# Performance work log

Measured on AMD Instinct MI355X. Metric: run time of the kernel, lower is better.

The kernel has to match this reference:

```python
import jax, jax.numpy as jnp
import numpy as np

# init_kwargs constants
K = 5                      # kernel_sz
SIGMA_SPATIAL = 2.0
SIGMA_INTENSITY = 0.1
KVAL = -1.0 / (2.0 * SIGMA_SPATIAL ** 2)        # kernel buffer value (same for all k^2 taps)
SIDIV = 1.0 / (2.0 * SIGMA_INTENSITY ** 2)      # sigma_intensity_div


def _extract_block(x, k):
    """F.unfold equivalent: (B,C,H,W) -> (B,H,W,k*k,C), SAME zero padding, row-major taps."""
    B, C, H, W = x.shape
    p = k // 2
    xp = jnp.pad(x, ((0, 0), (0, 0), (p, p), (p, p)))
    # fixed small loop over k*k taps (not a data-dim loop)
    pats = jnp.stack([xp[:, :, i:i + H, j:j + W] for i in range(k) for j in range(k)], axis=2)  # B,C,k2,H,W
    return jnp.transpose(pats, (0, 3, 4, 2, 1))  # B,H,W,k2,C


def setup_inputs() -> dict:
    key = jax.random.key(0)
    k1, k2 = jax.random.split(key)
    template = jax.random.uniform(k1, (1, 3, 1080, 1920), dtype=jnp.float32)
    vector_curr = jax.random.normal(k2, (1, 2, 1080, 1920), dtype=jnp.float32)
    return {"template": template, "vector_curr": vector_curr}


def reference(template, vector_curr):
    # inputs are float32, so cast() is a no-op
    compare_pix = jnp.transpose(template, (0, 2, 3, 1))[:, :, :, None, :]   # B,H,W,1,C
    compare_kernel = _extract_block(template, K)                            # B,H,W,k2,C
    intensity_diff = jnp.sum((compare_pix - compare_kernel) ** 2, axis=-1)  # B,H,W,k2
    coeff = jnp.clip(1.0 - jnp.abs(KVAL - intensity_diff * SIDIV), 0.0, 1.0)[..., None]  # B,H,W,k2,1
    vector_block = _extract_block(vector_curr, K)                           # B,H,W,k2,Cv
    num = jnp.sum(vector_block * coeff, axis=-2)                            # B,H,W,Cv
    den = jnp.sum(coeff, axis=-2)                                           # B,H,W,1
    out = (num / den).astype(jnp.float16)
    return jnp.transpose(out, (0, 3, 1, 2))                                  # B,Cv,H,W fp16
```

## Files before the change

kernel.cpp:

```cpp
#include <hip/hip_runtime.h>


#define IMG_H 1080
#define IMG_W 1920
#define IMG_HW (IMG_H * IMG_W)
#define TS_X 64
#define TS_Y 16
#define HALO_H 20
#define HALO_W 72
#define NCH 5
#define F4_PER_ROW 18
#define F4_PER_CH  (F4_PER_ROW * HALO_H)

typedef float f4u __attribute__((ext_vector_type(4), aligned(4)));

__global__ __launch_bounds__(256)
void jbf_kernel(const float* __restrict__ tpl,
                const float* __restrict__ vec,
                float* __restrict__ out) {
    constexpr float KVAL  = -0.125f;
    constexpr float SIDIV = 50.0f;

    __shared__ __align__(16) float smem[NCH][HALO_H][HALO_W];

    const int tid = threadIdx.x;
    const int x0  = blockIdx.x * TS_X;
    const int y0  = blockIdx.y * TS_Y;

    const bool interior = (blockIdx.x >= 1) & (blockIdx.x <= 28) &
                          (blockIdx.y >= 1) & (blockIdx.y <= 66);

    if (interior) {
        const int i0  = tid;
        const int i1  = tid + 256;
        const bool p1 = (i1 < F4_PER_CH);
        const int i1c = p1 ? i1 : 0;
        const int r0 = i0 / F4_PER_ROW, c0 = i0 - r0 * F4_PER_ROW;
        const int r1 = i1c / F4_PER_ROW, c1 = i1c - r1 * F4_PER_ROW;
        const int off0 = r0 * IMG_W + c0 * 4;
        const int off1 = r1 * IMG_W + c1 * 4;
        const int tl   = (y0 - 2) * IMG_W + (x0 - 2);

        f4u v[2 * NCH];
#pragma unroll
        for (int ch = 0; ch < NCH; ++ch) {
            const float* __restrict__ src =
                (ch < 3) ? (tpl + ch * IMG_HW) : (vec + (ch - 3) * IMG_HW);
            v[2 * ch]     = *(const f4u*)(src + tl + off0);
            v[2 * ch + 1] = *(const f4u*)(src + tl + off1);
        }
#pragma unroll
        for (int ch = 0; ch < NCH; ++ch) {
            float4* d0 = (float4*)&smem[ch][r0][c0 * 4];
            d0->x = v[2 * ch].x; d0->y = v[2 * ch].y;
            d0->z = v[2 * ch].z; d0->w = v[2 * ch].w;
            if (p1) {
                float4* d1 = (float4*)&smem[ch][r1][c1 * 4];
                d1->x = v[2 * ch + 1].x; d1->y = v[2 * ch + 1].y;
                d1->z = v[2 * ch + 1].z; d1->w = v[2 * ch + 1].w;
            }
        }
    } else {
#pragma unroll
        for (int c = 0; c < NCH; ++c) {
            const float* __restrict__ src =
                (c < 3) ? (tpl + c * IMG_HW) : (vec + (c - 3) * IMG_HW);
#pragma unroll
            for (int i = tid; i < HALO_H * HALO_W; i += 256) {
                const int r   = i / HALO_W;
                const int col = i - r * HALO_W;
                const int gy  = y0 + r - 2;
                const int gx  = x0 + col - 2;
                float val = 0.0f;
                if (gy >= 0 && gy < IMG_H && gx >= 0 && gx < IMG_W)
                    val = src[gy * IMG_W + gx];
                smem[c][r][col] = val;
            }
        }
    }
    __syncthreads();

    const int tx = tid & 15;
    const int ty = tid >> 4;
    const int lx = tx * 4;

    float num0[4] = {0.f, 0.f, 0.f, 0.f};
    float num1[4] = {0.f, 0.f, 0.f, 0.f};
    float den [4] = {0.f, 0.f, 0.f, 0.f};

    float c0[4], c1[4], c2[4];
#pragma unroll
    for (int px = 0; px < 4; ++px) {
        c0[px] = smem[0][ty + 2][lx + 2 + px];
        c1[px] = smem[1][ty + 2][lx + 2 + px];
        c2[px] = smem[2][ty + 2][lx + 2 + px];
    }

#pragma unroll
    for (int dy = 0; dy < 5; ++dy) {
        const int row = ty + dy;
        float4 a0 = *(const float4*)&smem[0][row][lx];
        float4 b0 = *(const float4*)&smem[0][row][lx + 4];
        float4 a1 = *(const float4*)&smem[1][row][lx];
        float4 b1 = *(const float4*)&smem[1][row][lx + 4];
        float4 a2 = *(const float4*)&smem[2][row][lx];
        float4 b2 = *(const float4*)&smem[2][row][lx + 4];
        float4 av0 = *(const float4*)&smem[3][row][lx];
        float4 bv0 = *(const float4*)&smem[3][row][lx + 4];
        float4 av1 = *(const float4*)&smem[4][row][lx];
        float4 bv1 = *(const float4*)&smem[4][row][lx + 4];

        const float w0[8]  = {a0.x, a0.y, a0.z, a0.w, b0.x, b0.y, b0.z, b0.w};
        const float w1[8]  = {a1.x, a1.y, a1.z, a1.w, b1.x, b1.y, b1.z, b1.w};
        const float w2[8]  = {a2.x, a2.y, a2.z, a2.w, b2.x, b2.y, b2.z, b2.w};
        const float wv0[8] = {av0.x, av0.y, av0.z, av0.w, bv0.x, bv0.y, bv0.z, bv0.w};
        const float wv1[8] = {av1.x, av1.y, av1.z, av1.w, bv1.x, bv1.y, bv1.z, bv1.w};

#pragma unroll
        for (int dx = 0; dx < 5; ++dx) {
#pragma unroll
            for (int px = 0; px < 4; ++px) {
                const int k = dx + px;
                const float d0 = c0[px] - w0[k];
                const float d1 = c1[px] - w1[k];
                const float d2 = c2[px] - w2[k];
                const float id = d0 * d0 + d1 * d1 + d2 * d2;
                const float t  = fabsf(KVAL - id * SIDIV);
                float coeff = 1.0f - t;
                coeff = fminf(fmaxf(coeff, 0.0f), 1.0f);
                num0[px] += wv0[k] * coeff;
                num1[px] += wv1[k] * coeff;
                den [px] += coeff;
            }
        }
    }

    const int gy = y0 + ty;
    if (gy < IMG_H) {
        const int gx = x0 + lx;
        float4 o0, o1;
        float r0 = __builtin_amdgcn_rcpf(den[0]);
        float r1 = __builtin_amdgcn_rcpf(den[1]);
        float r2 = __builtin_amdgcn_rcpf(den[2]);
        float r3 = __builtin_amdgcn_rcpf(den[3]);
        o0.x = num0[0] * r0; o0.y = num0[1] * r1; o0.z = num0[2] * r2; o0.w = num0[3] * r3;
        o1.x = num1[0] * r0; o1.y = num1[1] * r1; o1.z = num1[2] * r2; o1.w = num1[3] * r3;
        *(float4*)(out + (size_t)0 * IMG_HW + gy * IMG_W + gx) = o0;
        *(float4*)(out + (size_t)1 * IMG_HW + gy * IMG_W + gx) = o1;
    }
}

extern "C" void kernel_launch(void* const* d_in, const int* in_sizes, int n_in,
                              void* d_out, int out_size, void* d_ws, size_t ws_size,
                              hipStream_t stream) {
    const float* tpl = (const float*)d_in[0];
    const float* vec = (const float*)d_in[1];
    float* out = (float*)d_out;

    dim3 grid(IMG_W / TS_X, (IMG_H + TS_Y - 1) / TS_Y);
    jbf_kernel<<<grid, 256, 0, stream>>>(tpl, vec, out);
}
```

Before: 108.8 us.

## Compute two output rows per thread with taller tiles and simplified coefficient

Tiles grow to 30 rows; 240 threads each compute two vertically adjacent output rows and reuse each loaded LDS halo row for both. This cuts LDS reads per output and shrinks halo overhead, at the cost of 16 idle threads per block and higher register pressure under a 3-blocks occupancy hint. The coefficient is rewritten as max(0.875 - 50*id, 0), which equals the original clamp because id is nonnegative. The LDS row stride is padded to 76 floats, and the grid now divides the height exactly, so the row bounds check is gone.

```diff
diff --git a/kernel.cpp b/kernel.cpp
--- a/kernel.cpp
+++ b/kernel.cpp
@@ -5,59 +5,59 @@
 #define IMG_W 1920
 #define IMG_HW (IMG_H * IMG_W)
 #define TS_X 64
-#define TS_Y 16
-#define HALO_H 20
-#define HALO_W 72
+#define TS_Y 30
+#define HALO_H 34
+#define HALO_W 68
+#define LDS_W 76
 #define NCH 5
-#define F4_PER_ROW 18
-#define F4_PER_CH  (F4_PER_ROW * HALO_H)
+#define F4_PER_ROW 17
+#define F4_PER_CH (F4_PER_ROW * HALO_H)
 
 typedef float f4u __attribute__((ext_vector_type(4), aligned(4)));
 
-__global__ __launch_bounds__(256)
+__global__ __launch_bounds__(256, 3)
 void jbf_kernel(const float* __restrict__ tpl,
                 const float* __restrict__ vec,
                 float* __restrict__ out) {
-    constexpr float KVAL  = -0.125f;
     constexpr float SIDIV = 50.0f;
 
-    __shared__ __align__(16) float smem[NCH][HALO_H][HALO_W];
+    __shared__ __align__(16) float smem[NCH][HALO_H][LDS_W];
 
     const int tid = threadIdx.x;
-    const int x0  = blockIdx.x * TS_X;
-    const int y0  = blockIdx.y * TS_Y;
+    const int bx = blockIdx.x, by = blockIdx.y;
+    const int x0 = bx * TS_X;
+    const int y0 = by * TS_Y;
 
-    const bool interior = (blockIdx.x >= 1) & (blockIdx.x <= 28) &
-                          (blockIdx.y >= 1) & (blockIdx.y <= 66);
+    const bool interior = (bx >= 1) & (bx <= 28) & (by >= 1) & (by <= 34);
 
     if (interior) {
-        const int i0  = tid;
-        const int i1  = tid + 256;
-        const bool p1 = (i1 < F4_PER_CH);
-        const int i1c = p1 ? i1 : 0;
-        const int r0 = i0 / F4_PER_ROW, c0 = i0 - r0 * F4_PER_ROW;
-        const int r1 = i1c / F4_PER_ROW, c1 = i1c - r1 * F4_PER_ROW;
-        const int off0 = r0 * IMG_W + c0 * 4;
-        const int off1 = r1 * IMG_W + c1 * 4;
-        const int tl   = (y0 - 2) * IMG_W + (x0 - 2);
-
-        f4u v[2 * NCH];
+        const int tl = (y0 - 2) * IMG_W + (x0 - 2);
+        f4u v[15];
 #pragma unroll
         for (int ch = 0; ch < NCH; ++ch) {
             const float* __restrict__ src =
                 (ch < 3) ? (tpl + ch * IMG_HW) : (vec + (ch - 3) * IMG_HW);
-            v[2 * ch]     = *(const f4u*)(src + tl + off0);
-            v[2 * ch + 1] = *(const f4u*)(src + tl + off1);
+#pragma unroll
+            for (int it = 0; it < 3; ++it) {
+                int idx = tid + it * 256;
+                idx = (idx < F4_PER_CH) ? idx : 0;
+                const int r  = idx / F4_PER_ROW;
+                const int c4 = idx - r * F4_PER_ROW;
+                v[ch * 3 + it] = *(const f4u*)(src + tl + r * IMG_W + c4 * 4);
+            }
         }
 #pragma unroll
         for (int ch = 0; ch < NCH; ++ch) {
-            float4* d0 = (float4*)&smem[ch][r0][c0 * 4];
-            d0->x = v[2 * ch].x; d0->y = v[2 * ch].y;
-            d0->z = v[2 * ch].z; d0->w = v[2 * ch].w;
-            if (p1) {
-                float4* d1 = (float4*)&smem[ch][r1][c1 * 4];
-                d1->x = v[2 * ch + 1].x; d1->y = v[2 * ch + 1].y;
-                d1->z = v[2 * ch + 1].z; d1->w = v[2 * ch + 1].w;
+#pragma unroll
+            for (int it = 0; it < 3; ++it) {
+                const int idx = tid + it * 256;
+                if (idx < F4_PER_CH) {
+                    const int r  = idx / F4_PER_ROW;
+                    const int c4 = idx - r * F4_PER_ROW;
+                    float4* d = (float4*)&smem[ch][r][c4 * 4];
+                    d->x = v[ch * 3 + it].x; d->y = v[ch * 3 + it].y;
+                    d->z = v[ch * 3 + it].z; d->w = v[ch * 3 + it].w;
+                }
             }
         }
     } else {
@@ -65,7 +65,6 @@
         for (int c = 0; c < NCH; ++c) {
             const float* __restrict__ src =
                 (c < 3) ? (tpl + c * IMG_HW) : (vec + (c - 3) * IMG_HW);
-#pragma unroll
             for (int i = tid; i < HALO_H * HALO_W; i += 256) {
                 const int r   = i / HALO_W;
                 const int col = i - r * HALO_W;
@@ -80,73 +79,111 @@
     }
     __syncthreads();
 
-    const int tx = tid & 15;
-    const int ty = tid >> 4;
-    const int lx = tx * 4;
+    const int tx  = tid & 15;
+    const int tyq = tid >> 4;
 
-    float num0[4] = {0.f, 0.f, 0.f, 0.f};
-    float num1[4] = {0.f, 0.f, 0.f, 0.f};
-    float den [4] = {0.f, 0.f, 0.f, 0.f};
+    if (tyq < 15) {
+        const int lx = tx * 4;
+        const int rA = tyq * 2;
 
-    float c0[4], c1[4], c2[4];
+        float cA0[4], cA1[4], cA2[4], cB0[4], cB1[4], cB2[4];
+        {
+            const float4 a0 = *(const float4*)&smem[0][rA + 2][lx];
+            const float4 b0 = *(const float4*)&smem[0][rA + 2][lx + 4];
+            const float4 a1 = *(const float4*)&smem[1][rA + 2][lx];
+            const float4 b1 = *(const float4*)&smem[1][rA + 2][lx + 4];
+            const float4 a2 = *(const float4*)&smem[2][rA + 2][lx];
+            const float4 b2 = *(const float4*)&smem[2][rA + 2][lx + 4];
+            cA0[0] = a0.z; cA0[1] = a0.w; cA0[2] = b0.x; cA0[3] = b0.y;
+            cA1[0] = a1.z; cA1[1] = a1.w; cA1[2] = b1.x; cA1[3] = b1.y;
+            cA2[0] = a2.z; cA2[1] = a2.w; cA2[2] = b2.x; cA2[3] = b2.y;
+        }
+        {
+            const float4 a0 = *(const float4*)&smem[0][rA + 3][lx];
+            const float4 b0 = *(const float4*)&smem[0][rA + 3][lx + 4];
+            const float4 a1 = *(const float4*)&smem[1][rA + 3][lx];
+            const float4 b1 = *(const float4*)&smem[1][rA + 3][lx + 4];
+            const float4 a2 = *(const float4*)&smem[2][rA + 3][lx];
+            const float4 b2 = *(const float4*)&smem[2][rA + 3][lx + 4];
+            cB0[0] = a0.z; cB0[1] = a0.w; cB0[2] = b0.x; cB0[3] = b0.y;
+            cB1[0] = a1.z; cB1[1] = a1.w; cB1[2] = b1.x; cB1[3] = b1.y;
+            cB2[0] = a2.z; cB2[1] = a2.w; cB2[2] = b2.x; cB2[3] = b2.y;
+        }
+
+        float n0A[4] = {0.f, 0.f, 0.f, 0.f}, n1A[4] = {0.f, 0.f, 0.f, 0.f};
+        float n0B[4] = {0.f, 0.f, 0.f, 0.f}, n1B[4] = {0.f, 0.f, 0.f, 0.f};
+        float dnA[4] = {0.f, 0.f, 0.f, 0.f}, dnB[4] = {0.f, 0.f, 0.f, 0.f};
+
+        float w0[8], w1[8], w2[8], wv0[8], wv1[8];
+
+        auto acc_row = [&](const float (&c0)[4], const float (&c1)[4], const float (&c2)[4],
+                           float (&n0)[4], float (&n1)[4], float (&dn)[4]) {
 #pragma unroll
-    for (int px = 0; px < 4; ++px) {
-        c0[px] = smem[0][ty + 2][lx + 2 + px];
-        c1[px] = smem[1][ty + 2][lx + 2 + px];
-        c2[px] = smem[2][ty + 2][lx + 2 + px];
-    }
+            for (int dx = 0; dx < 5; ++dx) {
+#pragma unroll
+                for (int px = 0; px < 4; ++px) {
+                    const int k = dx + px;
+                    const float d0 = c0[px] - w0[k];
+                    const float d1 = c1[px] - w1[k];
+                    const float d2 = c2[px] - w2[k];
+                    const float id = fmaf(d0, d0, fmaf(d1, d1, d2 * d2));
+                    const float coeff = fmaxf(fmaf(id, -SIDIV, 0.875f), 0.0f);
+                    n0[px] = fmaf(wv0[k], coeff, n0[px]);
+                    n1[px] = fmaf(wv1[k], coeff, n1[px]);
+                    dn[px] += coeff;
+                }
+            }
+        };
 
 #pragma unroll
-    for (int dy = 0; dy < 5; ++dy) {
-        const int row = ty + dy;
-        float4 a0 = *(const float4*)&smem[0][row][lx];
-        float4 b0 = *(const float4*)&smem[0][row][lx + 4];
-        float4 a1 = *(const float4*)&smem[1][row][lx];
-        float4 b1 = *(const float4*)&smem[1][row][lx + 4];
-        float4 a2 = *(const float4*)&smem[2][row][lx];
-        float4 b2 = *(const float4*)&smem[2][row][lx + 4];
-        float4 av0 = *(const float4*)&smem[3][row][lx];
-        float4 bv0 = *(const float4*)&smem[3][row][lx + 4];
-        float4 av1 = *(const float4*)&smem[4][row][lx];
-        float4 bv1 = *(const float4*)&smem[4][row][lx + 4];
+        for (int r = 0; r < 6; ++r) {
+            const int hr = rA + r;
+            const float4 a0 = *(const float4*)&smem[0][hr][lx];
+            const float4 b0 = *(const float4*)&smem[0][hr][lx + 4];
+            const float4 a1 = *(const float4*)&smem[1][hr][lx];
+            const float4 b1 = *(const float4*)&smem[1][hr][lx + 4];
+            const float4 a2 = *(const float4*)&smem[2][hr][lx];
+            const float4 b2 = *(const float4*)&smem[2][hr][lx + 4];
+            const float4 av0 = *(const float4*)&smem[3][hr][lx];
+            const float4 bv0 = *(const float4*)&smem[3][hr][lx + 4];
+            const float4 av1 = *(const float4*)&smem[4][hr][lx];
+            const float4 bv1 = *(const float4*)&smem[4][hr][lx + 4];
 
-        const float w0[8]  = {a0.x, a0.y, a0.z, a0.w, b0.x, b0.y, b0.z, b0.w};
-        const float w1[8]  = {a1.x, a1.y, a1.z, a1.w, b1.x, b1.y, b1.z, b1.w};
-        const float w2[8]  = {a2.x, a2.y, a2.z, a2.w, b2.x, b2.y, b2.z, b2.w};
-        const float wv0[8] = {av0.x, av0.y, av0.z, av0.w, bv0.x, bv0.y, bv0.z, bv0.w};
-        const float wv1[8] = {av1.x, av1.y, av1.z, av1.w, bv1.x, bv1.y, bv1.z, bv1.w};
+            w0[0]=a0.x; w0[1]=a0.y; w0[2]=a0.z; w0[3]=a0.w; w0[4]=b0.x; w0[5]=b0.y; w0[6]=b0.z; w0[7]=b0.w;
+            w1[0]=a1.x; w1[1]=a1.y; w1[2]=a1.z; w1[3]=a1.w; w1[4]=b1.x; w1[5]=b1.y; w1[6]=b1.z; w1[7]=b1.w;
+            w2[0]=a2.x; w2[1]=a2.y; w2[2]=a2.z; w2[3]=a2.w; w2[4]=b2.x; w2[5]=b2.y; w2[6]=b2.z; w2[7]=b2.w;
+            wv0[0]=av0.x; wv0[1]=av0.y; wv0[2]=av0.z; wv0[3]=av0.w; wv0[4]=bv0.x; wv0[5]=bv0.y; wv0[6]=bv0.z; wv0[7]=bv0.w;
+            wv1[0]=av1.x; wv1[1]=av1.y; wv1[2]=av1.z; wv1[3]=av1.w; wv1[4]=bv1.x; wv1[5]=bv1.y; wv1[6]=bv1.z; wv1[7]=bv1.w;
 
-#pragma unroll
-        for (int dx = 0; dx < 5; ++dx) {
-#pragma unroll
-            for (int px = 0; px < 4; ++px) {
-                const int k = dx + px;
-                const float d0 = c0[px] - w0[k];
-                const float d1 = c1[px] - w1[k];
-                const float d2 = c2[px] - w2[k];
-                const float id = d0 * d0 + d1 * d1 + d2 * d2;
-                const float t  = fabsf(KVAL - id * SIDIV);
-                float coeff = 1.0f - t;
-                coeff = fminf(fmaxf(coeff, 0.0f), 1.0f);
-                num0[px] += wv0[k] * coeff;
-                num1[px] += wv1[k] * coeff;
-                den [px] += coeff;
-            }
+            if (r < 5) acc_row(cA0, cA1, cA2, n0A, n1A, dnA);
+            if (r > 0) acc_row(cB0, cB1, cB2, n0B, n1B, dnB);
         }
-    }
 
-    const int gy = y0 + ty;
-    if (gy < IMG_H) {
-        const int gx = x0 + lx;
-        float4 o0, o1;
-        float r0 = __builtin_amdgcn_rcpf(den[0]);
-        float r1 = __builtin_amdgcn_rcpf(den[1]);
-        float r2 = __builtin_amdgcn_rcpf(den[2]);
-        float r3 = __builtin_amdgcn_rcpf(den[3]);
-        o0.x = num0[0] * r0; o0.y = num0[1] * r1; o0.z = num0[2] * r2; o0.w = num0[3] * r3;
-        o1.x = num1[0] * r0; o1.y = num1[1] * r1; o1.z = num1[2] * r2; o1.w = num1[3] * r3;
-        *(float4*)(out + (size_t)0 * IMG_HW + gy * IMG_W + gx) = o0;
-        *(float4*)(out + (size_t)1 * IMG_HW + gy * IMG_W + gx) = o1;
+        const int gx  = x0 + lx;
+        const int gyA = y0 + rA;
+
+        float4 oA0, oA1, oB0, oB1;
+        {
+            const float r0 = __builtin_amdgcn_rcpf(dnA[0]);
+            const float r1 = __builtin_amdgcn_rcpf(dnA[1]);
+            const float r2 = __builtin_amdgcn_rcpf(dnA[2]);
+            const float r3 = __builtin_amdgcn_rcpf(dnA[3]);
+            oA0.x = n0A[0] * r0; oA0.y = n0A[1] * r1; oA0.z = n0A[2] * r2; oA0.w = n0A[3] * r3;
+            oA1.x = n1A[0] * r0; oA1.y = n1A[1] * r1; oA1.z = n1A[2] * r2; oA1.w = n1A[3] * r3;
+        }
+        {
+            const float r0 = __builtin_amdgcn_rcpf(dnB[0]);
+            const float r1 = __builtin_amdgcn_rcpf(dnB[1]);
+            const float r2 = __builtin_amdgcn_rcpf(dnB[2]);
+            const float r3 = __builtin_amdgcn_rcpf(dnB[3]);
+            oB0.x = n0B[0] * r0; oB0.y = n0B[1] * r1; oB0.z = n0B[2] * r2; oB0.w = n0B[3] * r3;
+            oB1.x = n1B[0] * r0; oB1.y = n1B[1] * r1; oB1.z = n1B[2] * r2; oB1.w = n1B[3] * r3;
+        }
+
+        *(float4*)(out + gyA * IMG_W + gx)                 = oA0;
+        *(float4*)(out + IMG_HW + gyA * IMG_W + gx)        = oA1;
+        *(float4*)(out + (gyA + 1) * IMG_W + gx)           = oB0;
+        *(float4*)(out + IMG_HW + (gyA + 1) * IMG_W + gx)  = oB1;
     }
 }
 
@@ -157,6 +194,6 @@
     const float* vec = (const float*)d_in[1];
     float* out = (float*)d_out;
 
-    dim3 grid(IMG_W / TS_X, (IMG_H + TS_Y - 1) / TS_Y);
+    dim3 grid(IMG_W / TS_X, IMG_H / TS_Y);
     jbf_kernel<<<grid, 256, 0, stream>>>(tpl, vec, out);
 }
```

New measurement: 222.6 us. +104.6%, slower.
